# Optimization experiments

Hardware: AMD Instinct MI355X
Metric: run time of the kernel (lower is better)

The kernel has to match this reference:

```python
import jax, jax.numpy as jnp
import numpy as np

N_NODE = 50000
D = 64
N_HEADS = 8
N_LAYERS = 2
NEG = -1e9
PAD = 0
STDV = 1.0 / np.sqrt(D)


def _l2norm(x, axis):
    n = jnp.sqrt(jnp.sum(x * x, axis=axis, keepdims=True))
    return x / jnp.maximum(n, 1e-12)


def _hgconv(x, theta, bias, edge_index):
    # PyG HypergraphConv (use_attention=False): out = D^-1 H B^-1 H^T (x @ theta) + bias
    xt = x @ theta
    node, hedge = edge_index[0], edge_index[1]
    ones = jnp.ones(node.shape[0], x.dtype)
    Bdeg = jax.ops.segment_sum(ones, hedge, num_segments=N_NODE)   # hyperedge degree
    Ddeg = jax.ops.segment_sum(ones, node, num_segments=N_NODE)    # node degree
    m = jax.ops.segment_sum(xt[node], hedge, num_segments=N_NODE)  # nodes -> hyperedges
    m = m * jnp.where(Bdeg > 0, 1.0 / Bdeg, 0.0)[:, None]
    out = jax.ops.segment_sum(m[hedge], node, num_segments=N_NODE) # hyperedges -> nodes
    out = out * jnp.where(Ddeg > 0, 1.0 / Ddeg, 0.0)[:, None]
    return out + bias


def _mha(x, w, pad_mask, reverse):
    # w: [4, D, D] -> q, k, v, out projections. reverse=True attends to future (triu).
    B, L, d = x.shape
    dk = d // N_HEADS
    split = lambda h: h.reshape(B, L, N_HEADS, dk).transpose(0, 2, 1, 3)
    q, k, v = split(x @ w[0]), split(x @ w[1]), split(x @ w[2])
    scores = jnp.einsum('bhid,bhjd->bhij', q, k) / jnp.sqrt(jnp.asarray(dk, x.dtype))
    tri = jnp.triu(jnp.ones((L, L), bool)) if reverse else jnp.tril(jnp.ones((L, L), bool))
    scores = jnp.where(tri[None, None], scores, NEG)
    scores = jnp.where(pad_mask[:, None, None, :], NEG, scores)
    attn = jax.nn.softmax(scores, axis=-1)
    out = jnp.einsum('bhij,bhjd->bhid', attn, v).transpose(0, 2, 1, 3).reshape(B, L, d)
    return out @ w[3], attn


def _prev_user_mask(seq):
    # scatter -1000 at every user id already seen up to position i (index 0 = PAD column)
    B, L = seq.shape
    tril = jnp.tril(jnp.ones((L, L), bool))
    idx = jnp.where(tril[None], seq[:, None, :], 0)                       # [B,L,L]
    idx = jnp.concatenate([idx, jnp.zeros((B, L, 1), idx.dtype)], axis=2)  # [B,L,L+1]
    b = jnp.arange(B)[:, None, None]
    i = jnp.arange(L)[None, :, None]
    return jnp.zeros((B, L, N_NODE), jnp.float32).at[b, i, idx].set(-1000.0)


def _hg_user(emb_table, gate_w, gate_b, att, att_m, theta, theta_b, edges):
    chans = []
    for c in range(3):
        x = emb_table * jax.nn.sigmoid(emb_table @ gate_w[c] + gate_b[c])  # self-gating
        acc, cur = x, x
        for k in range(N_LAYERS):
            cur = _hgconv(cur, theta[k], theta_b[k], edges[c])
            acc = acc + _l2norm(cur, axis=1)
        chans.append(acc / (N_LAYERS + 1))  # mean over [input, layer1, layer2]
    logits = jnp.stack([jnp.sum(att * (c @ att_m), axis=1) for c in chans], axis=1)  # [N,3]
    score = jax.nn.softmax(logits, axis=-1)
    return sum(score[:, i:i + 1] * chans[i] for i in range(3))


def setup_inputs() -> dict:
    key = jax.random.key(0)
    ks = jax.random.split(key, 20)
    u = lambda k, shp: jax.random.uniform(k, shp, jnp.float32, -STDV, STDV)
    B, L, E = 16, 50, 800000
    return {
        'input_seq': jax.random.randint(ks[0], (B, L), 0, N_NODE),
        'label_seq': jax.random.randint(ks[1], (B, L), 0, N_NODE),
        'input_time': jax.random.randint(ks[2], (B, L), 0, 100000),
        'label_time': jax.random.randint(ks[3], (B, L), 0, 100000),
        'edge_index_g': jax.random.randint(ks[4], (2, E), 0, N_NODE),
        'edge_index_i': jax.random.randint(ks[5], (2, E), 0, N_NODE),
        'edge_index_u': jax.random.randint(ks[6], (2, E), 0, N_NODE),
        'emb_table': u(ks[7], (N_NODE, D)),
        'gate_w': u(ks[8], (3, D, D)),
        'gate_b': u(ks[9], (3, D)),
        'att': u(ks[10], (D,)),
        'att_m': u(ks[11], (D, D)),
        'theta': u(ks[12], (N_LAYERS, D, D)),
        'theta_b': u(ks[13], (N_LAYERS, D)),
        'w_hist': u(ks[14], (4, D, D)),
        'w_fut': u(ks[15], (4, D, D)),
    }


def reference(input_seq, label_seq, input_time, label_time,
              edge_index_g, edge_index_i, edge_index_u,
              emb_table, gate_w, gate_b, att, att_m, theta, theta_b, w_hist, w_fut):
    # input_time / label_time are accepted but unused, as in the original forward.
    HG = _hg_user(emb_table, gate_w, gate_b, att, att_m, theta, theta_b,
                  (edge_index_g, edge_index_i, edge_index_u))
    pad_in = input_seq == PAD
    pad_lb = label_seq == PAD
    past_att_out, past_dist = _mha(HG[input_seq], w_hist, pad_in, reverse=False)
    fut_att_out, fut_dist = _mha(HG[label_seq], w_fut, pad_lb, reverse=True)
    output_past = (past_att_out @ HG.T + _prev_user_mask(input_seq)).reshape(-1, N_NODE)
    future_output = (fut_att_out @ HG.T).reshape(-1, N_NODE)
    return (output_past, future_output, past_dist, fut_dist,
            _l2norm(past_att_out, axis=1), _l2norm(fut_att_out, axis=1))
```

## Files before the change

kernel.cpp:

```cpp
#include <hip/hip_runtime.h>
#include <math.h>

#define N_NODE 50000
#define DD 64
#define NE 800000
#define BB 16
#define LL 50
#define NH 8
#define DK 8
#define NEGV -1e9f
#define NB 49
#define NBLK 256
#define EPB 3125

#define OFF_PDIST 80000000u
#define OFF_FDIST 80320000u
#define OFF_L2P 80640000u
#define OFF_L2F 80691200u

typedef unsigned short ushortt;
typedef __attribute__((ext_vector_type(8))) short bf16x8v;
typedef __attribute__((ext_vector_type(4))) float f32x4v;

__device__ __forceinline__ float b2f(ushortt h) { return __uint_as_float(((unsigned)h) << 16); }
__device__ __forceinline__ ushortt f2b(float f) {
    unsigned u = __float_as_uint(f);
    return (ushortt)((u + 0x7fffu + ((u >> 16) & 1u)) >> 16);
}
__device__ __forceinline__ void acc8(float* a, uint4 x) {
    a[0] += b2f((ushortt)(x.x)); a[1] += b2f((ushortt)(x.x >> 16));
    a[2] += b2f((ushortt)(x.y)); a[3] += b2f((ushortt)(x.y >> 16));
    a[4] += b2f((ushortt)(x.z)); a[5] += b2f((ushortt)(x.z >> 16));
    a[6] += b2f((ushortt)(x.w)); a[7] += b2f((ushortt)(x.w >> 16));
}
__device__ __forceinline__ uint4 pack8(const float* a) {
    uint4 w;
    w.x = (unsigned)f2b(a[0]) | ((unsigned)f2b(a[1]) << 16);
    w.y = (unsigned)f2b(a[2]) | ((unsigned)f2b(a[3]) << 16);
    w.z = (unsigned)f2b(a[4]) | ((unsigned)f2b(a[5]) << 16);
    w.w = (unsigned)f2b(a[6]) | ((unsigned)f2b(a[7]) << 16);
    return w;
}

__global__ void k_zero(float* p, int n) {
    int i = blockIdx.x * 256 + threadIdx.x;
    if (i < n) p[i] = 0.0f;
}

__global__ __launch_bounds__(256) void k_cnt(const int* __restrict__ eg,
                                             const int* __restrict__ ei,
                                             const int* __restrict__ eu,
                                             int* __restrict__ hist) {
    int c = blockIdx.y;
    const int* ed = (c == 0) ? eg : ((c == 1) ? ei : eu);
    int blk = blockIdx.x;
    __shared__ int lc[2 * NB];
    int tid = threadIdx.x;
    for (int j = tid; j < 2 * NB; j += 256) lc[j] = 0;
    __syncthreads();
    int e0 = blk * EPB;
    for (int i = e0 + tid; i < e0 + EPB; i += 256) {
        atomicAdd(&lc[ed[NE + i] >> 10], 1);
        atomicAdd(&lc[NB + (ed[i] >> 10)], 1);
    }
    __syncthreads();
    for (int j = tid; j < 2 * NB; j += 256) {
        int side = (j >= NB);
        int b = side ? (j - NB) : j;
        hist[(((side * 3 + c) * NB) + b) * NBLK + blk] = lc[j];
    }
}

__global__ __launch_bounds__(256) void k_scanH(int* __restrict__ hist, int* __restrict__ bb) {
    int t6 = blockIdx.x;
    int* h = hist + t6 * NB * NBLK;
    __shared__ int part[256];
    int tid = threadIdx.x;
    const int CH = (NB * NBLK) / 256;
    int base = tid * CH;
    int s = 0;
    for (int i = 0; i < CH; i++) s += h[base + i];
    part[tid] = s;
    __syncthreads();
    for (int o = 1; o < 256; o <<= 1) {
        int v = (tid >= o) ? part[tid - o] : 0;
        __syncthreads();
        part[tid] += v;
        __syncthreads();
    }
    int run = (tid == 0) ? 0 : part[tid - 1];
    for (int i = 0; i < CH; i++) {
        int idx = base + i;
        int v = h[idx];
        if ((idx & (NBLK - 1)) == 0) bb[t6 * (NB + 1) + (idx >> 8)] = run;
        h[idx] = run;
        run += v;
    }
    if (tid == 255) bb[t6 * (NB + 1) + NB] = run;
}

__global__ __launch_bounds__(256) void k_part2(const int* __restrict__ eg,
                                               const int* __restrict__ ei,
                                               const int* __restrict__ eu,
                                               const int* __restrict__ hist,
                                               unsigned* __restrict__ poolB,
                                               unsigned* __restrict__ poolD) {
    int c = blockIdx.y;
    const int* ed = (c == 0) ? eg : ((c == 1) ? ei : eu);
    int blk = blockIdx.x;
    __shared__ int curB[NB], curD[NB];
    int tid = threadIdx.x;
    for (int j = tid; j < NB; j += 256) {
        curB[j] = hist[(((0 * 3 + c) * NB) + j) * NBLK + blk];
        curD[j] = hist[(((1 * 3 + c) * NB) + j) * NBLK + blk];
    }
    __syncthreads();
    unsigned* pB = poolB + c * 800000;
    unsigned* pD = poolD + c * 800000;
    int e0 = blk * EPB;
    for (int i = e0 + tid; i < e0 + EPB; i += 256) {
        int n = ed[i], h = ed[NE + i];
        int pb = atomicAdd(&curB[h >> 10], 1);
        pB[pb] = ((unsigned)h << 16) | (unsigned)n;
        int pd = atomicAdd(&curD[n >> 10], 1);
        pD[pd] = ((unsigned)n << 16) | (unsigned)h;
    }
}

__global__ __launch_bounds__(256) void k_bucket(const unsigned* __restrict__ poolB,
                                                const unsigned* __restrict__ poolD,
                                                const int* __restrict__ bb,
                                                int* __restrict__ nbrB3, int* __restrict__ nbrD3,
                                                int* __restrict__ offB3, int* __restrict__ offD3,
                                                float* __restrict__ invB3, float* __restrict__ invD3) {
    int b = blockIdx.x, c = blockIdx.y, side = blockIdx.z;
    const unsigned* pool = (side ? poolD : poolB) + c * 800000;
    int* nbr = (side ? nbrD3 : nbrB3) + c * 800000;
    int* off = (side ? offD3 : offB3) + c * 50001;
    float* inv = (side ? invD3 : invB3) + c * 50000;
    int t6 = side * 3 + c;
    int s0 = bb[t6 * (NB + 1) + b], s1 = bb[t6 * (NB + 1) + b + 1];
    int baseSeg = b << 10;
    __shared__ int cnt[1024];
    __shared__ int ofs[1024];
    __shared__ int part[256];
    int tid = threadIdx.x;
    for (int j = tid; j < 1024; j += 256) cnt[j] = 0;
    __syncthreads();
    for (int i = s0 + tid; i < s1; i += 256)
        atomicAdd(&cnt[(pool[i] >> 16) & 1023], 1);
    __syncthreads();
    int t4 = tid * 4;
    int a0 = cnt[t4], a1 = cnt[t4 + 1], a2 = cnt[t4 + 2], a3 = cnt[t4 + 3];
    part[tid] = a0 + a1 + a2 + a3;
    __syncthreads();
    for (int o = 1; o < 256; o <<= 1) {
        int v = (tid >= o) ? part[tid - o] : 0;
        __syncthreads();
        part[tid] += v;
        __syncthreads();
    }
    int excl = (tid == 0) ? 0 : part[tid - 1];
    ofs[t4] = excl;
    ofs[t4 + 1] = excl + a0;
    ofs[t4 + 2] = excl + a0 + a1;
    ofs[t4 + 3] = excl + a0 + a1 + a2;
    __syncthreads();
    for (int ls = tid; ls < 1024; ls += 256) {
        int seg = baseSeg + ls;
        if (seg < N_NODE) {
            off[seg] = s0 + ofs[ls];
            inv[seg] = cnt[ls] ? 1.0f / (float)cnt[ls] : 0.0f;
        }
    }
    if (b == NB - 1 && tid == 0) off[N_NODE] = NE;
    __syncthreads();
    for (int i = s0 + tid; i < s1; i += 256) {
        unsigned u = pool[i];
        int ls = (u >> 16) & 1023;
        int p = atomicAdd(&ofs[ls], 1);
        nbr[s0 + p] = (int)(u & 0xFFFFu);
    }
}

__global__ __launch_bounds__(256) void k_gateX(const float* __restrict__ emb,
                                               const float* __restrict__ gate_w,
                                               const float* __restrict__ gate_b,
                                               float* __restrict__ acc3,
                                               ushortt* __restrict__ xt3) {
    int c = blockIdx.y;
    const float* W = gate_w + c * 4096;
    const float* bias = gate_b + c * 64;
    float* acc = acc3 + (size_t)c * 3200000;
    ushortt* xt = xt3 + (size_t)c * 3200000;
    __shared__ float sW[64 * 64];
    __shared__ float sx[4][64];
    int tid = threadIdx.x;
    for (int i = tid; i < 4096; i += 256) sW[i] = W[i];
    int r = tid >> 6;
    int d = tid & 63;
    int n = blockIdx.x * 4 + r;
    sx[r][d] = emb[n * DD + d];
    __syncthreads();
    float a = bias[d];
#pragma unroll
    for (int k = 0; k < 64; k++) a += sx[r][k] * sW[k * 64 + d];
    float x = sx[r][d] * (1.0f / (1.0f + expf(-a)));
    acc[n * DD + d] = x;
    xt[n * DD + d] = f2b(x);
}

__global__ __launch_bounds__(256) void k_gathB3(const ushortt* __restrict__ xt3,
                                                const int* __restrict__ offB3,
                                                const int* __restrict__ nbrB3,
                                                const float* __restrict__ invB3,
                                                ushortt* __restrict__ m3) {
    int c = blockIdx.y;
    const ushortt* src = xt3 + (size_t)c * 3200000;
    const int* off = offB3 + c * 50001;
    const int* nbr = nbrB3 + c * 800000;
    const float* invSeg = invB3 + c * 50000;
    ushortt* dst = m3 + (size_t)c * 3200000;
    int seg = blockIdx.x * 4 + (threadIdx.x >> 6);
    int lane = threadIdx.x & 63;
    int sub = lane >> 3;
    int c8 = lane & 7;
    int s = off[seg], e = off[seg + 1];
    float a[8] = {0.f, 0.f, 0.f, 0.f, 0.f, 0.f, 0.f, 0.f};
    for (int i = s + sub; i < e; i += 8) {
        uint4 x = ((const uint4*)(src + (size_t)nbr[i] * DD))[c8];
        acc8(a, x);
    }
#pragma unroll
    for (int j = 0; j < 8; j++) {
        a[j] += __shfl_xor(a[j], 8, 64);
        a[j] += __shfl_xor(a[j], 16, 64);
        a[j] += __shfl_xor(a[j], 32, 64);
    }
    if (sub == 0) {
        float sc = invSeg[seg];
        float b[8];
#pragma unroll
        for (int j = 0; j < 8; j++) b[j] = a[j] * sc;
        ((uint4*)(dst + (size_t)seg * DD))[c8] = pack8(b);
    }
}

template <int WRITE_XT>
__global__ __launch_bounds__(256) void k_gathD3f(const ushortt* __restrict__ m3,
                                                 const int* __restrict__ offD3,
                                                 const int* __restrict__ nbrD3,
                                                 const float* __restrict__ invD3,
                                                 const float* __restrict__ theta,
                                                 const float* __restrict__ theta_b,
                                                 float* __restrict__ acc3,
                                                 ushortt* __restrict__ xt3) {
    int c = blockIdx.y;
    const ushortt* m = m3 + (size_t)c * 3200000;
    const int* off = offD3 + c * 50001;
    const int* nbr = nbrD3 + c * 800000;
    const float* invD = invD3 + c * 50000;
    float* acc = acc3 + (size_t)c * 3200000;
    ushortt* xt = xt3 + (size_t)c * 3200000;

    __shared__ float sTh[64 * 64];
    __shared__ float sx[4][64];
    __shared__ float sb[64];
    int tid = threadIdx.x;
    for (int i = tid; i < 4096; i += 256) sTh[i] = theta[i];
    if (tid < 64) sb[tid] = theta_b[tid];

    int w = tid >> 6;
    int seg = blockIdx.x * 4 + w;
    int lane = tid & 63;
    int sub = lane >> 3;
    int c8 = lane & 7;
    int s = off[seg], e = off[seg + 1];
    float a[8] = {0.f, 0.f, 0.f, 0.f, 0.f, 0.f, 0.f, 0.f};
    for (int i = s + sub; i < e; i += 8) {
        uint4 x = ((const uint4*)(m + (size_t)nbr[i] * DD))[c8];
        acc8(a, x);
    }
#pragma unroll
    for (int j = 0; j < 8; j++) {
        a[j] += __shfl_xor(a[j], 8, 64);
        a[j] += __shfl_xor(a[j], 16, 64);
        a[j] += __shfl_xor(a[j], 32, 64);
    }
    if (sub == 0) {
        float iD = invD[seg];
#pragma unroll
        for (int j = 0; j < 8; j++) sx[w][c8 * 8 + j] = a[j] * iD;
    }
    __syncthreads();

    int d = lane;
    float v = sb[d];
#pragma unroll
    for (int k = 0; k < 64; k++) v += sx[w][k] * sTh[k * 64 + d];
    float ss = v * v;
#pragma unroll
    for (int o = 32; o; o >>= 1) ss += __shfl_xor(ss, o, 64);
    float nr = fmaxf(sqrtf(ss), 1e-12f);
    size_t idx = (size_t)seg * DD + d;
    acc[idx] += v / nr;
    if (WRITE_XT) xt[idx] = f2b(v);
}

__global__ __launch_bounds__(256) void k_comb(const float* __restrict__ a0,
                                              const float* __restrict__ a1,
                                              const float* __restrict__ a2,
                                              const float* __restrict__ att_m,
                                              const float* __restrict__ att,
                                              float* __restrict__ HG,
                                              ushortt* __restrict__ HG16) {
    __shared__ float svv[64];
    int tid = threadIdx.x;
    if (tid < 64) {
        float s = 0.f;
        for (int k = 0; k < 64; k++) s += att_m[tid * 64 + k] * att[k];
        svv[tid] = s;
    }
    __syncthreads();
    int r = tid >> 6;
    int d = tid & 63;
    int n = blockIdx.x * 4 + r;
    float x0 = a0[n * DD + d], x1 = a1[n * DD + d], x2 = a2[n * DD + d];
    float vd = svv[d];
    float l0 = x0 * vd, l1 = x1 * vd, l2 = x2 * vd;
#pragma unroll
    for (int o = 32; o; o >>= 1) {
        l0 += __shfl_xor(l0, o, 64);
        l1 += __shfl_xor(l1, o, 64);
        l2 += __shfl_xor(l2, o, 64);
    }
    l0 *= (1.0f / 3.0f); l1 *= (1.0f / 3.0f); l2 *= (1.0f / 3.0f);
    float mx = fmaxf(l0, fmaxf(l1, l2));
    float e0 = expf(l0 - mx), e1 = expf(l1 - mx), e2 = expf(l2 - mx);
    float inv = 1.0f / (e0 + e1 + e2);
    float hv = (e0 * x0 + e1 * x1 + e2 * x2) * inv * (1.0f / 3.0f);
    HG[n * DD + d] = hv;
    HG16[n * DD + d] = f2b(hv);
}

__global__ __launch_bounds__(256) void k_attn(const float* __restrict__ HG,
                                              const int* __restrict__ iseq,
                                              const int* __restrict__ lseq,
                                              const float* __restrict__ w_hist,
                                              const float* __restrict__ w_fut,
                                              float* __restrict__ dout,
                                              ushortt* __restrict__ attout16,
                                              float* __restrict__ attoutF) {
    int b = blockIdx.x;
    int dir = blockIdx.y;
    const int* seq = (dir == 0) ? iseq : lseq;
    const float* W = (dir == 0) ? w_hist : w_fut;
    float* dist = dout + ((dir == 0) ? OFF_PDIST : OFF_FDIST);

    __shared__ float sX[LL * 64];
    __shared__ float sQ[LL * 64];
    __shared__ float sK[LL * 64];
    __shared__ float sV[LL * 64];
    __shared__ float sS[LL * LL];
    __shared__ float sInv[64];
    __shared__ int sseq[LL];

    int tid = threadIdx.x;
    if (tid < LL) sseq[tid] = seq[b * LL + tid];
    __syncthreads();
    for (int idx = tid; idx < LL * 64; idx += 256) {
        int i = idx >> 6, d = idx & 63;
        sX[idx] = HG[sseq[i] * DD + d];
    }
    __syncthreads();
    for (int idx = tid; idx < LL * 64; idx += 256) {
        int i = idx >> 6, d = idx & 63;
        float q = 0, k = 0, v = 0;
        for (int kk = 0; kk < 64; kk++) {
            float x = sX[i * 64 + kk];
            q += x * W[kk * 64 + d];
            k += x * W[4096 + kk * 64 + d];
            v += x * W[8192 + kk * 64 + d];
        }
        sQ[idx] = q; sK[idx] = k; sV[idx] = v;
    }
    __syncthreads();
    for (int idx = tid; idx < LL * 64; idx += 256) sX[idx] = 0.0f;
    __syncthreads();

    const float scale = 0.35355339059327373f;
    for (int h = 0; h < NH; h++) {
        for (int idx = tid; idx < LL * LL; idx += 256) {
            int i = idx / LL, j = idx % LL;
            float s = 0;
#pragma unroll
            for (int d = 0; d < DK; d++) s += sQ[i * 64 + h * 8 + d] * sK[j * 64 + h * 8 + d];
            s *= scale;
            bool allowed = (dir == 0) ? (j <= i) : (j >= i);
            if (!allowed) s = NEGV;
            if (sseq[j] == 0) s = NEGV;
            sS[idx] = s;
        }
        __syncthreads();
        if (tid < LL) {
            int i = tid;
            float mx = -INFINITY;
            for (int j = 0; j < LL; j++) mx = fmaxf(mx, sS[i * LL + j]);
            float sum = 0;
            for (int j = 0; j < LL; j++) {
                float e = expf(sS[i * LL + j] - mx);
                sS[i * LL + j] = e;
                sum += e;
            }
            float inv = 1.0f / sum;
            for (int j = 0; j < LL; j++) {
                float p = sS[i * LL + j] * inv;
                sS[i * LL + j] = p;
                dist[((b * NH + h) * LL + i) * LL + j] = p;
            }
        }
        __syncthreads();
        for (int idx = tid; idx < LL * DK; idx += 256) {
            int i = idx / DK, d8 = idx % DK;
            float o = 0;
            for (int j = 0; j < LL; j++) o += sS[i * LL + j] * sV[j * 64 + h * 8 + d8];
            sX[i * 64 + h * 8 + d8] = o;
        }
        __syncthreads();
    }
    for (int idx = tid; idx < LL * 64; idx += 256) {
        int i = idx >> 6, d = idx & 63;
        float o = 0;
        for (int kk = 0; kk < 64; kk++) o += sX[i * 64 + kk] * W[3 * 4096 + kk * 64 + d];
        sQ[idx] = o;
        int row = dir * 800 + b * LL + i;
        attout16[row * 64 + d] = f2b(o);
        if (attoutF) attoutF[row * 64 + d] = o;
    }
    __syncthreads();
    if (tid < 64) {
        float s = 0;
        for (int l = 0; l < LL; l++) {
            float x = sQ[l * 64 + tid];
            s += x * x;
        }
        sInv[tid] = 1.0f / fmaxf(sqrtf(s), 1e-12f);
    }
    __syncthreads();
    float* ol2 = dout + ((dir == 0) ? OFF_L2P : OFF_L2F) + b * LL * 64;
    for (int idx = tid; idx < LL * 64; idx += 256) {
        int d = idx & 63;
        ol2[idx] = sQ[idx] * sInv[d];
    }
}

__global__ __launch_bounds__(256) void k_bigmm_mfma(const ushortt* __restrict__ A16,
                                                    const ushortt* __restrict__ HG16,
                                                    float* __restrict__ out) {
    int lane = threadIdx.x & 63;
    int w = threadIdx.x >> 6;
    int rt = blockIdx.y * 4 + w;
    int colBase = blockIdx.x * 256;
    int lrow = lane & 15;
    int kb = (lane >> 4) * 8;
    int arow = rt * 16 + lrow;
    bf16x8v a0 = *(const bf16x8v*)(A16 + (size_t)arow * 64 + kb);
    bf16x8v a1 = *(const bf16x8v*)(A16 + (size_t)arow * 64 + kb + 32);
#pragma unroll 4
    for (int ct = 0; ct < 16; ct++) {
        int cb = colBase + ct * 16;
        if (cb >= N_NODE) break;
        int col = cb + lrow;
        bf16x8v b0 = *(const bf16x8v*)(HG16 + (size_t)col * 64 + kb);
        bf16x8v b1 = *(const bf16x8v*)(HG16 + (size_t)col * 64 + kb + 32);
        f32x4v acc = {0.f, 0.f, 0.f, 0.f};
        acc = __builtin_amdgcn_mfma_f32_16x16x32_bf16(a0, b0, acc, 0, 0, 0);
        acc = __builtin_amdgcn_mfma_f32_16x16x32_bf16(a1, b1, acc, 0, 0, 0);
        size_t base = (size_t)(rt * 16 + (lane >> 4) * 4) * 50000 + col;
        out[base] = acc[0];
        out[base + 50000] = acc[1];
        out[base + 100000] = acc[2];
        out[base + 150000] = acc[3];
    }
}

__global__ __launch_bounds__(64) void k_mask(const int* __restrict__ iseq,
                                             float* __restrict__ out) {
    int row = blockIdx.x;
    int b = row / LL, i = row % LL;
    __shared__ int s[LL];
    int tid = threadIdx.x;
    if (tid < LL) s[tid] = iseq[b * LL + tid];
    __syncthreads();
    float* o = out + (size_t)row * 50000;
    if (tid == 0) o[0] -= 1000.0f;
    if (tid < LL && tid <= i) {
        int c = s[tid];
        if (c > 0 && c < N_NODE) {
            bool first = true;
            for (int j = 0; j < tid; j++)
                if (s[j] == c) { first = false; break; }
            if (first) o[c] -= 1000.0f;
        }
    }
}

__global__ void k_deg(const int* __restrict__ node, const int* __restrict__ hedge,
                      float* __restrict__ Ddeg, float* __restrict__ Bdeg) {
    int e = blockIdx.x * 256 + threadIdx.x;
    if (e < NE) {
        atomicAdd(&Ddeg[node[e]], 1.0f);
        atomicAdd(&Bdeg[hedge[e]], 1.0f);
    }
}

__global__ void k_inv(float* a, int n) {
    int i = blockIdx.x * 256 + threadIdx.x;
    if (i < n) a[i] = (a[i] > 0.0f) ? (1.0f / a[i]) : 0.0f;
}

__global__ __launch_bounds__(256) void k_scat(const float* __restrict__ src,
                                              const int* __restrict__ gidx,
                                              const int* __restrict__ sidx,
                                              const float* __restrict__ scale,
                                              float* __restrict__ dst) {
    int e = blockIdx.x * 4 + (threadIdx.x >> 6);
    int d = threadIdx.x & 63;
    if (e >= NE) return;
    int g = gidx[e];
    int s = sidx[e];
    float v = src[g * DD + d];
    if (scale) v *= scale[g];
    atomicAdd(&dst[s * DD + d], v);
}

__global__ __launch_bounds__(256) void k_fin(float* __restrict__ cur,
                                             const float* __restrict__ invD,
                                             const float* __restrict__ bias,
                                             float* __restrict__ acc) {
    int r = threadIdx.x >> 6;
    int d = threadIdx.x & 63;
    int n = blockIdx.x * 4 + r;
    float v = cur[n * DD + d] * invD[n] + bias[d];
    cur[n * DD + d] = v;
    float s = v * v;
#pragma unroll
    for (int o = 32; o; o >>= 1) s += __shfl_xor(s, o, 64);
    float nr = fmaxf(sqrtf(s), 1e-12f);
    acc[n * DD + d] += v / nr;
}

__global__ __launch_bounds__(256) void k_gate(const float* __restrict__ emb,
                                              const float* __restrict__ W,
                                              const float* __restrict__ bias,
                                              float* __restrict__ cur,
                                              float* __restrict__ acc) {
    __shared__ float sW[64 * 64];
    __shared__ float sx[4][64];
    int tid = threadIdx.x;
    for (int i = tid; i < 4096; i += 256) sW[i] = W[i];
    int r = tid >> 6;
    int d = tid & 63;
    int n = blockIdx.x * 4 + r;
    sx[r][d] = emb[n * DD + d];
    __syncthreads();
    float a = bias[d];
#pragma unroll
    for (int k = 0; k < 64; k++) a += sx[r][k] * sW[k * 64 + d];
    float x = sx[r][d] * (1.0f / (1.0f + expf(-a)));
    cur[n * DD + d] = x;
    acc[n * DD + d] = x;
}

__global__ __launch_bounds__(256) void k_mm64(const float* __restrict__ X,
                                              const float* __restrict__ W,
                                              float* __restrict__ Y) {
    __shared__ float sW[64 * 64];
    __shared__ float sx[4][64];
    int tid = threadIdx.x;
    for (int i = tid; i < 4096; i += 256) sW[i] = W[i];
    int r = tid >> 6;
    int d = tid & 63;
    int n = blockIdx.x * 4 + r;
    sx[r][d] = X[n * DD + d];
    __syncthreads();
    float a = 0.0f;
#pragma unroll
    for (int k = 0; k < 64; k++) a += sx[r][k] * sW[k * 64 + d];
    Y[n * DD + d] = a;
}

__global__ __launch_bounds__(256) void k_bigmm5(const float* __restrict__ A,
                                                const float* __restrict__ HG,
                                                float* __restrict__ out) {
    int col = blockIdx.x * 256 + threadIdx.x;
    int r0 = blockIdx.y * 400;
    bool ok = (col < N_NODE);
    float4 h[16];
    const float4* hp = (const float4*)(HG + (size_t)(ok ? col : 0) * 64);
#pragma unroll
    for (int t = 0; t < 16; t++) h[t] = hp[t];
    if (!ok) return;
    for (int r = 0; r < 400; r++) {
        int row = r0 + r;
        const float* ar = A + (size_t)row * 64;
        float q0 = 0.f, q1 = 0.f, q2 = 0.f, q3 = 0.f;
#pragma unroll
        for (int t = 0; t < 16; t++) {
            q0 += ar[4 * t + 0] * h[t].x;
            q1 += ar[4 * t + 1] * h[t].y;
            q2 += ar[4 * t + 2] * h[t].z;
            q3 += ar[4 * t + 3] * h[t].w;
        }
        out[(size_t)row * 50000 + col] = (q0 + q1) + (q2 + q3);
    }
}

extern "C" void kernel_launch(void* const* d_in, const int* in_sizes, int n_in,
                              void* d_out, int out_size, void* d_ws, size_t ws_size,
                              hipStream_t stream) {
    const int* input_seq = (const int*)d_in[0];
    const int* label_seq = (const int*)d_in[1];
    const int* eg = (const int*)d_in[4];
    const int* ei = (const int*)d_in[5];
    const int* eu = (const int*)d_in[6];
    const float* emb = (const float*)d_in[7];
    const float* gate_w = (const float*)d_in[8];
    const float* gate_b = (const float*)d_in[9];
    const float* att = (const float*)d_in[10];
    const float* att_m = (const float*)d_in[11];
    const float* theta = (const float*)d_in[12];
    const float* theta_b = (const float*)d_in[13];
    const float* w_hist = (const float*)d_in[14];
    const float* w_fut = (const float*)d_in[15];

    float* out = (float*)d_out;
    float* ws = (float*)d_ws;

    const size_t HGF = 3200000;
    const int HISTN = 6 * NB * NBLK;
    const size_t needA = (HGF + 150000 + 150000 +
                          (size_t)(HISTN + 6 * (NB + 1) + 64) +
                          300006 + 4 * 2400000 +
                          2 * 2400000 +
                          3 * HGF +
                          HGF / 2 + 51200 + 1024) * 4;

    if (ws_size >= needA) {
        size_t o = 0;
        float* HG = ws + o; o += HGF;
        float* invB3 = ws + o; o += 150000;
        float* invD3 = ws + o; o += 150000;
        int* hist = (int*)(ws + o); o += HISTN;
        int* bbarr = (int*)(ws + o); o += 6 * (NB + 1) + 64;
        int* offB3 = (int*)(ws + o); o += 150003;
        int* offD3 = (int*)(ws + o); o += 150003 + 2;
        int* nbrB3 = (int*)(ws + o); o += 2400000;
        int* nbrD3 = (int*)(ws + o); o += 2400000;
        unsigned* poolB = (unsigned*)(ws + o); o += 2400000;
        unsigned* poolD = (unsigned*)(ws + o); o += 2400000;
        ushortt* xt3 = (ushortt*)(ws + o); o += 4800000;
        ushortt* m3 = (ushortt*)(ws + o); o += 4800000;
        float* acc3 = ws + o; o += 3 * HGF;
        ushortt* HG16 = (ushortt*)(ws + o); o += HGF / 2;
        ushortt* A16 = (ushortt*)(ws + o); o += 51200;

        dim3 pg(NBLK, 3);
        k_cnt<<<pg, 256, 0, stream>>>(eg, ei, eu, hist);
        k_scanH<<<6, 256, 0, stream>>>(hist, bbarr);
        k_part2<<<pg, 256, 0, stream>>>(eg, ei, eu, hist, poolB, poolD);
        dim3 dg(NB, 3, 2);
        k_bucket<<<dg, 256, 0, stream>>>(poolB, poolD, bbarr, nbrB3, nbrD3,
                                         offB3, offD3, invB3, invD3);

        dim3 ng3(12500, 3);
        k_gateX<<<ng3, 256, 0, stream>>>(emb, gate_w, gate_b, acc3, xt3);
        k_gathB3<<<ng3, 256, 0, stream>>>(xt3, offB3, nbrB3, invB3, m3);
        k_gathD3f<1><<<ng3, 256, 0, stream>>>(m3, offD3, nbrD3, invD3,
                                              theta, theta_b, acc3, xt3);
        k_gathB3<<<ng3, 256, 0, stream>>>(xt3, offB3, nbrB3, invB3, m3);
        k_gathD3f<0><<<ng3, 256, 0, stream>>>(m3, offD3, nbrD3, invD3,
                                              theta + 4096, theta_b + 64, acc3, xt3);

        k_comb<<<12500, 256, 0, stream>>>(acc3, acc3 + HGF, acc3 + 2 * HGF,
                                          att_m, att, HG, HG16);
        dim3 ag(BB, 2);
        k_attn<<<ag, 256, 0, stream>>>(HG, input_seq, label_seq, w_hist, w_fut,
                                       out, A16, nullptr);
        dim3 bg(196, 25);
        k_bigmm_mfma<<<bg, 256, 0, stream>>>(A16, HG16, out);
        k_mask<<<BB * LL, 64, 0, stream>>>(input_seq, out);
    } else {
        float* HG = ws;
        float* invB = HG + HGF;
        float* invD = invB + 50000;
        if (ws_size < (HGF + 100000 + 64) * 4) {
            HG = out + 36550000u;
            invB = HG + HGF;
            invD = invB + 50000;
        }
        float* trans = out;
        float* acc0 = trans;
        float* acc1 = trans + HGF;
        float* acc2 = trans + 2 * HGF;
        float* cur = trans + 3 * HGF;
        float* xt = trans + 4 * HGF;
        float* m = trans + 5 * HGF;
        float* accs[3] = {acc0, acc1, acc2};
        const int* edges[3] = {eg, ei, eu};
        for (int c = 0; c < 3; c++) {
            const int* node = edges[c];
            const int* hedge = edges[c] + NE;
            k_zero<<<(100000 + 255) / 256, 256, 0, stream>>>(invB, 100000);
            k_deg<<<(NE + 255) / 256, 256, 0, stream>>>(node, hedge, invD, invB);
            k_inv<<<(100000 + 255) / 256, 256, 0, stream>>>(invB, 100000);
            k_gate<<<12500, 256, 0, stream>>>(emb, gate_w + c * 4096, gate_b + c * 64, cur, accs[c]);
            for (int k = 0; k < 2; k++) {
                k_mm64<<<12500, 256, 0, stream>>>(cur, theta + k * 4096, xt);
                k_zero<<<12500, 256, 0, stream>>>(m, (int)HGF);
                k_scat<<<NE / 4, 256, 0, stream>>>(xt, node, hedge, nullptr, m);
                k_zero<<<12500, 256, 0, stream>>>(cur, (int)HGF);
                k_scat<<<NE / 4, 256, 0, stream>>>(m, hedge, node, invB, cur);
                k_fin<<<12500, 256, 0, stream>>>(cur, invD, theta_b + k * 64, accs[c]);
            }
        }
        k_comb<<<12500, 256, 0, stream>>>(acc0, acc1, acc2, att_m, att, HG, (ushortt*)m);
        dim3 ag(BB, 2);
        k_attn<<<ag, 256, 0, stream>>>(HG, input_seq, label_seq, w_hist, w_fut,
                                       out, (ushortt*)(m + HGF), xt);
        dim3 bg5(196, 4);
        k_bigmm5<<<bg5, 256, 0, stream>>>(xt, HG, out);
        k_mask<<<BB * LL, 64, 0, stream>>>(input_seq, out);
    }
}
```

Measured before the change: 845.1 us.

## Prefetch gather loads, warp-parallel softmax, LDS-staged coalesced output in big matmul

The segment-gather kernels now issue the next neighbor row load before accumulating the current one, a software prefetch that hides memory latency. The attention softmax moves from one thread per row to one wavefront per row using shuffle reductions. The big output matmul stages each 16x256 tile in shared memory and then writes 16-byte nontemporal row-contiguous stores, in place of scattered 4-byte stores. Its grid grows to one 16-row tile per block. The cost is extra LDS traffic and a barrier in exchange for coalesced writes to the large output.

```diff
diff --git a/kernel.cpp b/kernel.cpp
--- a/kernel.cpp
+++ b/kernel.cpp
@@ -227,8 +227,14 @@
     int c8 = lane & 7;
     int s = off[seg], e = off[seg + 1];
     float a[8] = {0.f, 0.f, 0.f, 0.f, 0.f, 0.f, 0.f, 0.f};
-    for (int i = s + sub; i < e; i += 8) {
+    int i = s + sub;
+    if (i < e) {
         uint4 x = ((const uint4*)(src + (size_t)nbr[i] * DD))[c8];
+        for (i += 8; i < e; i += 8) {
+            uint4 nx = ((const uint4*)(src + (size_t)nbr[i] * DD))[c8];
+            acc8(a, x);
+            x = nx;
+        }
         acc8(a, x);
     }
 #pragma unroll
@@ -277,8 +283,14 @@
     int c8 = lane & 7;
     int s = off[seg], e = off[seg + 1];
     float a[8] = {0.f, 0.f, 0.f, 0.f, 0.f, 0.f, 0.f, 0.f};
-    for (int i = s + sub; i < e; i += 8) {
+    int i = s + sub;
+    if (i < e) {
         uint4 x = ((const uint4*)(m + (size_t)nbr[i] * DD))[c8];
+        for (i += 8; i < e; i += 8) {
+            uint4 nx = ((const uint4*)(m + (size_t)nbr[i] * DD))[c8];
+            acc8(a, x);
+            x = nx;
+        }
         acc8(a, x);
     }
 #pragma unroll
@@ -366,6 +378,8 @@
     __shared__ int sseq[LL];
 
     int tid = threadIdx.x;
+    int w = tid >> 6;
+    int lane = tid & 63;
     if (tid < LL) sseq[tid] = seq[b * LL + tid];
     __syncthreads();
     for (int idx = tid; idx < LL * 64; idx += 256) {
@@ -402,21 +416,19 @@
             sS[idx] = s;
         }
         __syncthreads();
-        if (tid < LL) {
-            int i = tid;
-            float mx = -INFINITY;
-            for (int j = 0; j < LL; j++) mx = fmaxf(mx, sS[i * LL + j]);
-            float sum = 0;
-            for (int j = 0; j < LL; j++) {
-                float e = expf(sS[i * LL + j] - mx);
-                sS[i * LL + j] = e;
-                sum += e;
-            }
-            float inv = 1.0f / sum;
-            for (int j = 0; j < LL; j++) {
-                float p = sS[i * LL + j] * inv;
-                sS[i * LL + j] = p;
-                dist[((b * NH + h) * LL + i) * LL + j] = p;
+        for (int i = w; i < LL; i += 4) {
+            float v = (lane < LL) ? sS[i * LL + lane] : -INFINITY;
+            float mx = v;
+#pragma unroll
+            for (int o = 32; o; o >>= 1) mx = fmaxf(mx, __shfl_xor(mx, o, 64));
+            float e = (lane < LL) ? expf(v - mx) : 0.0f;
+            float sum = e;
+#pragma unroll
+            for (int o = 32; o; o >>= 1) sum += __shfl_xor(sum, o, 64);
+            float p = e / sum;
+            if (lane < LL) {
+                sS[i * LL + lane] = p;
+                dist[((b * NH + h) * LL + i) * LL + lane] = p;
             }
         }
         __syncthreads();
@@ -457,30 +469,45 @@
 __global__ __launch_bounds__(256) void k_bigmm_mfma(const ushortt* __restrict__ A16,
                                                     const ushortt* __restrict__ HG16,
                                                     float* __restrict__ out) {
-    int lane = threadIdx.x & 63;
-    int w = threadIdx.x >> 6;
-    int rt = blockIdx.y * 4 + w;
+    __shared__ float sO[16][260];
+    int tid = threadIdx.x;
+    int lane = tid & 63;
+    int w = tid >> 6;
+    int rt = blockIdx.y;
     int colBase = blockIdx.x * 256;
     int lrow = lane & 15;
     int kb = (lane >> 4) * 8;
     int arow = rt * 16 + lrow;
     bf16x8v a0 = *(const bf16x8v*)(A16 + (size_t)arow * 64 + kb);
     bf16x8v a1 = *(const bf16x8v*)(A16 + (size_t)arow * 64 + kb + 32);
-#pragma unroll 4
-    for (int ct = 0; ct < 16; ct++) {
-        int cb = colBase + ct * 16;
-        if (cb >= N_NODE) break;
-        int col = cb + lrow;
-        bf16x8v b0 = *(const bf16x8v*)(HG16 + (size_t)col * 64 + kb);
-        bf16x8v b1 = *(const bf16x8v*)(HG16 + (size_t)col * 64 + kb + 32);
+#pragma unroll
+    for (int ct = 0; ct < 4; ct++) {
+        int lc = w * 64 + ct * 16 + lrow;
+        int col = colBase + lc;
+        int colc = (col < N_NODE) ? col : 0;
+        bf16x8v b0 = *(const bf16x8v*)(HG16 + (size_t)colc * 64 + kb);
+        bf16x8v b1 = *(const bf16x8v*)(HG16 + (size_t)colc * 64 + kb + 32);
         f32x4v acc = {0.f, 0.f, 0.f, 0.f};
         acc = __builtin_amdgcn_mfma_f32_16x16x32_bf16(a0, b0, acc, 0, 0, 0);
         acc = __builtin_amdgcn_mfma_f32_16x16x32_bf16(a1, b1, acc, 0, 0, 0);
-        size_t base = (size_t)(rt * 16 + (lane >> 4) * 4) * 50000 + col;
-        out[base] = acc[0];
-        out[base + 50000] = acc[1];
-        out[base + 100000] = acc[2];
-        out[base + 150000] = acc[3];
+        int r0 = (lane >> 4) * 4;
+#pragma unroll
+        for (int j = 0; j < 4; j++) sO[r0 + j][lc] = acc[j];
+    }
+    __syncthreads();
+#pragma unroll
+    for (int j = 0; j < 4; j++) {
+        int r = w * 4 + j;
+        int row = rt * 16 + r;
+        int c0 = colBase + lane * 4;
+        f32x4v v = {sO[r][lane * 4], sO[r][lane * 4 + 1],
+                    sO[r][lane * 4 + 2], sO[r][lane * 4 + 3]};
+        if (c0 + 3 < N_NODE) {
+            __builtin_nontemporal_store(v, (f32x4v*)(out + (size_t)row * 50000 + c0));
+        } else {
+            for (int t = 0; t < 4; t++)
+                if (c0 + t < N_NODE) out[(size_t)row * 50000 + c0 + t] = v[t];
+        }
     }
 }
 
@@ -687,7 +714,7 @@
         dim3 ag(BB, 2);
         k_attn<<<ag, 256, 0, stream>>>(HG, input_seq, label_seq, w_hist, w_fut,
                                        out, A16, nullptr);
-        dim3 bg(196, 25);
+        dim3 bg(196, 100);
         k_bigmm_mfma<<<bg, 256, 0, stream>>>(A16, HG16, out);
         k_mask<<<BB * LL, 64, 0, stream>>>(input_seq, out);
     } else {
```

New measurement: 829.6 us. About the same (-1.8%).
